# Performance work log

Hardware: AMD Instinct MI355X
Metric: run time of the kernel (lower is better)

Reference implementation:

```python
import jax, jax.numpy as jnp
import numpy as np

N_STATE = 1024
N_HEAD = 16
H_DIM = N_STATE // N_HEAD  # 64
NUM_ROT = 32
BASE = 10000.0
B, S = 4, 8192


def setup_inputs() -> dict:
    key = jax.random.key(0)
    k1, k2, k3 = jax.random.split(key, 3)
    x = jax.random.normal(k1, (B, S, N_STATE), dtype=jnp.float32)
    # learned params (use non-trivial values so the math is exercised)
    thetas = 0.1 * jax.random.normal(k2, (NUM_ROT,), dtype=jnp.float32)
    rotation_matrix = jnp.eye(H_DIM, dtype=jnp.float32) + 0.02 * jax.random.normal(k3, (H_DIM, H_DIM), dtype=jnp.float32)
    # buffer: inv_freq = 1 / base^(arange(0, h_dim, 2)/h_dim)
    inv_freq = 1.0 / (BASE ** (jnp.arange(0, H_DIM, 2, dtype=jnp.float32) / H_DIM))
    return {"x": x, "thetas": thetas, "rotation_matrix": rotation_matrix, "inv_freq": inv_freq}


def reference(x, thetas, rotation_matrix, inv_freq):
    batch, seq_len, n_state = x.shape
    h_dim = rotation_matrix.shape[0]
    n_head = n_state // h_dim
    num_rot = thetas.shape[0]

    xf = x.reshape(-1, h_dim)  # [B*S*n_head, h_dim]
    # Sequential Givens rotations: x @ G_k only mixes columns i and j.
    for k in range(num_rot):
        i, j = k % h_dim, (k + 1) % h_dim
        c = jnp.cos(thetas[k])
        s = jnp.sin(thetas[k])
        xi, xj = xf[:, i], xf[:, j]
        xf = xf.at[:, i].set(xi * c + xj * s).at[:, j].set(-xi * s + xj * c)
    xf = xf @ rotation_matrix
    xr = xf.reshape(batch, seq_len, n_head, h_dim)

    # RoPE-style sin/cos mixing (split-even/odd, concat halves as in source)
    pos = jnp.arange(seq_len, dtype=jnp.float32)
    sinusoid = pos[:, None] * inv_freq[None, :]          # [S, h_dim/2]
    sin = jnp.sin(sinusoid)[None, :, None, :]            # [1,S,1,h_dim/2]
    cos = jnp.cos(sinusoid)[None, :, None, :]
    x1, x2 = xr[..., ::2], xr[..., 1::2]
    out = jnp.concatenate([x1 * cos - x2 * sin, x1 * sin + x2 * cos], axis=-1)
    return out.reshape(batch, seq_len, n_state)
```

## Files before the change

### kernel.cpp

```cpp
#include <hip/hip_runtime.h>
#include <hip/hip_bf16.h>


#define N_TILES 32768
#define N_BLOCKS (N_TILES / 4)

typedef __attribute__((ext_vector_type(8))) short short8;
typedef __attribute__((ext_vector_type(4))) float f32x4;

__device__ __forceinline__ unsigned short f2bf_bits(float f) {
  return __bfloat16_as_ushort(__float2bfloat16(f));
}

__global__ __launch_bounds__(64) void prep_kernel(
    const float* __restrict__ thetas,
    const float* __restrict__ R,
    short* __restrict__ Bws) {
  const int t = threadIdx.x;
  float col[64];
#pragma unroll
  for (int d = 0; d < 64; ++d) col[d] = R[d * 64 + t];
#pragma unroll
  for (int k = 31; k >= 0; --k) {
    float th = thetas[k];
    float ck = cosf(th), sk = sinf(th);
    float a = col[k], b = col[k + 1];
    col[k]     = ck * a - sk * b;
    col[k + 1] = sk * a + ck * b;
  }
  __shared__ float Ml[64][64];
#pragma unroll
  for (int d = 0; d < 64; ++d) Ml[d][t] = col[d];
  __syncthreads();

  short8* Bp = (short8*)Bws;
  const int cb = t & 15, kg = t >> 4;
#pragma unroll
  for (int s = 0; s < 2; ++s) {
#pragma unroll
    for (int nt = 0; nt < 4; ++nt) {
      const int c2 = cb + 16 * nt;
      const int pc = (c2 < 32) ? (2 * c2) : (2 * (c2 - 32) + 1);
      short8 hf;
#pragma unroll
      for (int e = 0; e < 8; ++e) {
        const int k = s * 32 + kg * 8 + e;
        hf[e] = (short)f2bf_bits(Ml[k][pc]);
      }
      Bp[(s * 4 + nt) * 64 + t] = hf;
    }
  }
}

__global__ void rope_mfma(
    const float* __restrict__ x,
    const float* __restrict__ inv_freq,
    const short* __restrict__ Bws,
    float* __restrict__ out) {
  const int lane = threadIdx.x & 63;
  const int wid = threadIdx.x >> 6;
  const int cb = lane & 15;
  const int kg = lane >> 4;

  const int tile = (int)blockIdx.x * 4 + wid;
  const size_t rb = (size_t)tile * 16;

  __shared__ alignas(16) float stage[4][16 * 64];
  float* st = stage[wid];

  const f32x4* xbase = (const f32x4*)(x + rb * 64);
  f32x4 v0 = xbase[lane];
  f32x4 v1 = xbase[64 + lane];
  f32x4 v2 = xbase[128 + lane];
  f32x4 v3 = xbase[192 + lane];

  const short8* Bp = (const short8*)Bws;
  short8 bh[8];
#pragma unroll
  for (int i = 0; i < 8; ++i) bh[i] = Bp[i * 64 + lane];

  const int pos = tile & 8191;
  float sv0, cv0, sv1, cv1;
  __sincosf((float)pos * inv_freq[cb], &sv0, &cv0);
  __sincosf((float)pos * inv_freq[cb + 16], &sv1, &cv1);

  {
    const int r0 = lane >> 4;
    const int c16 = lane & 15;
    f32x4 vv[4] = {v0, v1, v2, v3};
#pragma unroll
    for (int j = 0; j < 4; ++j) {
      const int row = j * 4 + r0;
      *(f32x4*)&st[row * 64 + (((c16 ^ row) & 15) << 2)] = vv[j];
    }
  }

  float af[2][8];
#pragma unroll
  for (int s = 0; s < 2; ++s) {
#pragma unroll
    for (int t2 = 0; t2 < 2; ++t2) {
      const int ch = s * 8 + kg * 2 + t2;
      f32x4 q = *(const f32x4*)&st[cb * 64 + (((ch ^ cb) & 15) << 2)];
      af[s][t2 * 4 + 0] = q.x;
      af[s][t2 * 4 + 1] = q.y;
      af[s][t2 * 4 + 2] = q.z;
      af[s][t2 * 4 + 3] = q.w;
    }
  }

  short8 ah[2], al[2];
#pragma unroll
  for (int s = 0; s < 2; ++s) {
#pragma unroll
    for (int e = 0; e < 8; ++e) {
      float f = af[s][e];
      __hip_bfloat16 h = __float2bfloat16(f);
      ah[s][e] = (short)__bfloat16_as_ushort(h);
      al[s][e] = (short)f2bf_bits(f - __bfloat162float(h));
    }
  }

  f32x4 acc[4];
#pragma unroll
  for (int nt = 0; nt < 4; ++nt) acc[nt] = (f32x4){0.f, 0.f, 0.f, 0.f};
#pragma unroll
  for (int s = 0; s < 2; ++s) {
#pragma unroll
    for (int nt = 0; nt < 4; ++nt) {
      acc[nt] = __builtin_amdgcn_mfma_f32_16x16x32_bf16(ah[s], bh[s * 4 + nt], acc[nt], 0, 0, 0);
      acc[nt] = __builtin_amdgcn_mfma_f32_16x16x32_bf16(al[s], bh[s * 4 + nt], acc[nt], 0, 0, 0);
    }
  }

#pragma unroll
  for (int nt = 0; nt < 4; ++nt) {
    const float cvx = (nt & 1) ? cv1 : cv0;
    const float ssv = ((nt & 1) ? sv1 : sv0) * ((nt < 2) ? -1.f : 1.f);
    const int chunk = (cb >> 2) + 4 * nt;
    const int c1i = cb & 3;
#pragma unroll
    for (int r = 0; r < 4; ++r) {
      const int lrow = kg * 4 + r;
      float y = acc[nt][r];
      float p = acc[nt ^ 2][r];
      st[lrow * 64 + ((chunk ^ lrow) << 2) + c1i] = fmaf(p, ssv, y * cvx);
    }
  }
  asm volatile("s_waitcnt lgkmcnt(0)");

#pragma unroll
  for (int i = 0; i < 4; ++i) {
    const int g = i * 4 + kg;
    const f32x4 v = *(const f32x4*)&st[g * 64 + ((cb ^ g) << 2)];
    __builtin_nontemporal_store(v, (f32x4*)(out + (rb + g) * 64) + cb);
  }
}

extern "C" void kernel_launch(void* const* d_in, const int* in_sizes, int n_in,
                              void* d_out, int out_size, void* d_ws, size_t ws_size,
                              hipStream_t stream) {
  const float* x        = (const float*)d_in[0];
  const float* thetas   = (const float*)d_in[1];
  const float* R        = (const float*)d_in[2];
  const float* inv_freq = (const float*)d_in[3];

  prep_kernel<<<1, 64, 0, stream>>>(thetas, R, (short*)d_ws);
  rope_mfma<<<N_BLOCKS, 256, 0, stream>>>(x, inv_freq, (const short*)d_ws, (float*)d_out);
}
```

Measured before the change: 54.21 us.

## Process eight tiles per wave with register prefetch and LDS-staged weights

Each wave now loops over eight consecutive 16-row tiles instead of one. It prefetches the next tile's input into registers while computing the current one, and double-buffers the LDS staging area. The bf16 weight fragments are copied once per block into shared memory, and the per-lane inv_freq values are hoisted out of the loop. This amortises the per-wave setup and B loads and overlaps global loads with compute. The cost is 8x fewer blocks, more LDS per block, and a new launch bound that may limit occupancy.

```diff
diff --git a/kernel.cpp b/kernel.cpp
--- a/kernel.cpp
+++ b/kernel.cpp
@@ -2,8 +2,9 @@
 #include <hip/hip_bf16.h>
 
 
+#define TOKENS_PER_WAVE 8
 #define N_TILES 32768
-#define N_BLOCKS (N_TILES / 4)
+#define N_BLOCKS (N_TILES / (4 * TOKENS_PER_WAVE))
 
 typedef __attribute__((ext_vector_type(8))) short short8;
 typedef __attribute__((ext_vector_type(4))) float f32x4;
@@ -52,7 +53,7 @@
   }
 }
 
-__global__ void rope_mfma(
+__global__ __launch_bounds__(256, 4) void rope_mfma(
     const float* __restrict__ x,
     const float* __restrict__ inv_freq,
     const short* __restrict__ Bws,
@@ -62,98 +63,126 @@
   const int cb = lane & 15;
   const int kg = lane >> 4;
 
-  const int tile = (int)blockIdx.x * 4 + wid;
-  const size_t rb = (size_t)tile * 16;
+  const int tile0 = ((int)blockIdx.x * 4 + wid) * TOKENS_PER_WAVE;
 
-  __shared__ alignas(16) float stage[4][16 * 64];
-  float* st = stage[wid];
+  __shared__ alignas(16) float stage[4][2][16 * 64];
+  __shared__ alignas(16) short8 Btab[8 * 64];
 
-  const f32x4* xbase = (const f32x4*)(x + rb * 64);
-  f32x4 v0 = xbase[lane];
-  f32x4 v1 = xbase[64 + lane];
-  f32x4 v2 = xbase[128 + lane];
-  f32x4 v3 = xbase[192 + lane];
+  f32x4 pb[4];
+  {
+    const f32x4* xb = (const f32x4*)x + (size_t)tile0 * 256;
+#pragma unroll
+    for (int j = 0; j < 4; ++j) pb[j] = xb[j * 64 + lane];
+  }
 
-  const short8* Bp = (const short8*)Bws;
+  {
+    const f32x4* Bg = (const f32x4*)Bws;
+    f32x4* Bl = (f32x4*)Btab;
+    const int i = threadIdx.x;
+    Bl[i] = Bg[i];
+    Bl[i + 256] = Bg[i + 256];
+  }
+  __syncthreads();
+
   short8 bh[8];
 #pragma unroll
-  for (int i = 0; i < 8; ++i) bh[i] = Bp[i * 64 + lane];
+  for (int i = 0; i < 8; ++i) bh[i] = Btab[i * 64 + lane];
 
-  const int pos = tile & 8191;
-  float sv0, cv0, sv1, cv1;
-  __sincosf((float)pos * inv_freq[cb], &sv0, &cv0);
-  __sincosf((float)pos * inv_freq[cb + 16], &sv1, &cv1);
+  const float iv0 = inv_freq[cb];
+  const float iv1 = inv_freq[cb + 16];
 
-  {
-    const int r0 = lane >> 4;
-    const int c16 = lane & 15;
-    f32x4 vv[4] = {v0, v1, v2, v3};
 #pragma unroll
-    for (int j = 0; j < 4; ++j) {
-      const int row = j * 4 + r0;
-      *(f32x4*)&st[row * 64 + (((c16 ^ row) & 15) << 2)] = vv[j];
+  for (int t = 0; t < TOKENS_PER_WAVE; ++t) {
+    const int tile = tile0 + t;
+    const size_t rb = (size_t)tile * 16;
+    float* st = stage[wid][t & 1];
+
+    f32x4 va[4];
+#pragma unroll
+    for (int j = 0; j < 4; ++j) va[j] = pb[j];
+    if (t + 1 < TOKENS_PER_WAVE) {
+      const f32x4* xn = (const f32x4*)x + (size_t)(tile + 1) * 256;
+#pragma unroll
+      for (int j = 0; j < 4; ++j) pb[j] = xn[j * 64 + lane];
     }
-  }
 
-  float af[2][8];
+    const int pos = tile & 8191;
+    float sv0, cv0, sv1, cv1;
+    __sincosf((float)pos * iv0, &sv0, &cv0);
+    __sincosf((float)pos * iv1, &sv1, &cv1);
+
+    {
+      const int r0 = lane >> 4;
+      const int c16 = lane & 15;
 #pragma unroll
-  for (int s = 0; s < 2; ++s) {
+      for (int j = 0; j < 4; ++j) {
+        const int row = j * 4 + r0;
+        *(f32x4*)&st[row * 64 + (((c16 ^ row) & 15) << 2)] = va[j];
+      }
+    }
+    asm volatile("" ::: "memory");
+
+    float af[2][8];
 #pragma unroll
-    for (int t2 = 0; t2 < 2; ++t2) {
-      const int ch = s * 8 + kg * 2 + t2;
-      f32x4 q = *(const f32x4*)&st[cb * 64 + (((ch ^ cb) & 15) << 2)];
-      af[s][t2 * 4 + 0] = q.x;
-      af[s][t2 * 4 + 1] = q.y;
-      af[s][t2 * 4 + 2] = q.z;
-      af[s][t2 * 4 + 3] = q.w;
+    for (int s = 0; s < 2; ++s) {
+#pragma unroll
+      for (int t2 = 0; t2 < 2; ++t2) {
+        const int ch = s * 8 + kg * 2 + t2;
+        f32x4 q = *(const f32x4*)&st[cb * 64 + (((ch ^ cb) & 15) << 2)];
+        af[s][t2 * 4 + 0] = q.x;
+        af[s][t2 * 4 + 1] = q.y;
+        af[s][t2 * 4 + 2] = q.z;
+        af[s][t2 * 4 + 3] = q.w;
+      }
     }
-  }
 
-  short8 ah[2], al[2];
+    short8 ah[2], al[2];
 #pragma unroll
-  for (int s = 0; s < 2; ++s) {
+    for (int s = 0; s < 2; ++s) {
 #pragma unroll
-    for (int e = 0; e < 8; ++e) {
-      float f = af[s][e];
-      __hip_bfloat16 h = __float2bfloat16(f);
-      ah[s][e] = (short)__bfloat16_as_ushort(h);
-      al[s][e] = (short)f2bf_bits(f - __bfloat162float(h));
+      for (int e = 0; e < 8; ++e) {
+        float f = af[s][e];
+        __hip_bfloat16 h = __float2bfloat16(f);
+        ah[s][e] = (short)__bfloat16_as_ushort(h);
+        al[s][e] = (short)f2bf_bits(f - __bfloat162float(h));
+      }
     }
-  }
 
-  f32x4 acc[4];
+    f32x4 acc[4];
 #pragma unroll
-  for (int nt = 0; nt < 4; ++nt) acc[nt] = (f32x4){0.f, 0.f, 0.f, 0.f};
+    for (int nt = 0; nt < 4; ++nt) acc[nt] = (f32x4){0.f, 0.f, 0.f, 0.f};
 #pragma unroll
-  for (int s = 0; s < 2; ++s) {
+    for (int s = 0; s < 2; ++s) {
+#pragma unroll
+      for (int nt = 0; nt < 4; ++nt) {
+        acc[nt] = __builtin_amdgcn_mfma_f32_16x16x32_bf16(ah[s], bh[s * 4 + nt], acc[nt], 0, 0, 0);
+        acc[nt] = __builtin_amdgcn_mfma_f32_16x16x32_bf16(al[s], bh[s * 4 + nt], acc[nt], 0, 0, 0);
+      }
+    }
+
 #pragma unroll
     for (int nt = 0; nt < 4; ++nt) {
-      acc[nt] = __builtin_amdgcn_mfma_f32_16x16x32_bf16(ah[s], bh[s * 4 + nt], acc[nt], 0, 0, 0);
-      acc[nt] = __builtin_amdgcn_mfma_f32_16x16x32_bf16(al[s], bh[s * 4 + nt], acc[nt], 0, 0, 0);
+      const float cvx = (nt & 1) ? cv1 : cv0;
+      const float ssv = ((nt & 1) ? sv1 : sv0) * ((nt < 2) ? -1.f : 1.f);
+      const int chunk = (cb >> 2) + 4 * nt;
+      const int c1i = cb & 3;
+#pragma unroll
+      for (int r = 0; r < 4; ++r) {
+        const int lrow = kg * 4 + r;
+        float y = acc[nt][r];
+        float p = acc[nt ^ 2][r];
+        st[lrow * 64 + ((chunk ^ lrow) << 2) + c1i] = fmaf(p, ssv, y * cvx);
+      }
     }
-  }
+    asm volatile("s_waitcnt lgkmcnt(0)" ::: "memory");
 
 #pragma unroll
-  for (int nt = 0; nt < 4; ++nt) {
-    const float cvx = (nt & 1) ? cv1 : cv0;
-    const float ssv = ((nt & 1) ? sv1 : sv0) * ((nt < 2) ? -1.f : 1.f);
-    const int chunk = (cb >> 2) + 4 * nt;
-    const int c1i = cb & 3;
-#pragma unroll
-    for (int r = 0; r < 4; ++r) {
-      const int lrow = kg * 4 + r;
-      float y = acc[nt][r];
-      float p = acc[nt ^ 2][r];
-      st[lrow * 64 + ((chunk ^ lrow) << 2) + c1i] = fmaf(p, ssv, y * cvx);
+    for (int i = 0; i < 4; ++i) {
+      const int g = i * 4 + kg;
+      const f32x4 v = *(const f32x4*)&st[g * 64 + ((cb ^ g) << 2)];
+      __builtin_nontemporal_store(v, (f32x4*)(out + (rb + g) * 64) + cb);
     }
-  }
-  asm volatile("s_waitcnt lgkmcnt(0)");
-
-#pragma unroll
-  for (int i = 0; i < 4; ++i) {
-    const int g = i * 4 + kg;
-    const f32x4 v = *(const f32x4*)&st[g * 64 + ((cb ^ g) << 2)];
-    __builtin_nontemporal_store(v, (f32x4*)(out + (rb + g) * 64) + cb);
+    asm volatile("" ::: "memory");
   }
 }
 
```

Result: no change. 54.85 us (+1.2%).
